# Kernel tuning notes

Measured on AMD Instinct MI355X. Metric: run time of the kernel, lower is better.

## Reference

```python
import jax, jax.numpy as jnp
import numpy as np

N_NODES, N_EDGES, IN_DIM = 100000, 1600000, 64


def setup_inputs() -> dict:
    key = jax.random.key(0)
    k1, k2, k3, k4, k5 = jax.random.split(key, 5)
    h = jax.random.normal(k1, (N_NODES, IN_DIM), dtype=jnp.float32)
    # per-node degree normalizer, e.g. 1/sqrt(deg); positive values in (0,1]
    d = jax.random.uniform(k2, (N_NODES,), dtype=jnp.float32, minval=0.05, maxval=1.0)
    src = jax.random.randint(k3, (N_EDGES,), 0, N_NODES, dtype=jnp.int32)
    dst = jax.random.randint(k4, (N_EDGES,), 0, N_NODES, dtype=jnp.int32)
    # xavier_normal with gain=1.414 for Linear(2*in_dim -> 1)
    xavier_std = 1.414 * np.sqrt(2.0 / (2 * IN_DIM + 1))
    gate_w = jax.random.normal(k5, (1, 2 * IN_DIM), dtype=jnp.float32) * xavier_std
    gate_b = jnp.zeros((1,), dtype=jnp.float32)
    return {"h": h, "d": d, "gate_w": gate_w, "gate_b": gate_b, "src": src, "dst": dst}


def reference(h, d, gate_w, gate_b, src, dst):
    """FAGCN layer forward (dropout in eval mode = identity).

    a_e = tanh(gate([h_dst ; h_src]))        per-edge scalar gate
    e_e = d_dst * d_src * a_e                degree-scaled edge weight
    z_v = sum_{e: dst(e)=v} h_src(e) * e_e   u_mul_e + sum aggregation
    """
    N, D = h.shape
    # gate concat order is [dst, src]; split the [1, 2D] weight so the per-edge
    # GEMV becomes two per-node GEMVs followed by a gather-add (same math).
    w_dst, w_src = gate_w[0, :D], gate_w[0, D:]
    s_dst = h @ w_dst  # [N]
    s_src = h @ w_src  # [N]
    a = jnp.tanh(s_dst[dst] + s_src[src] + gate_b[0])  # [E]
    e = d[dst] * d[src] * a                            # [E] (dropout = identity in eval)
    msg = h[src] * e[:, None]                          # [E, D] gathered messages
    z = jax.ops.segment_sum(msg, dst, num_segments=N)  # [N, D]
    return z
```

## Files before the change

### kernel.cpp

```cpp
#include <hip/hip_runtime.h>

#define D 64
#define NB 2048
#define NPB 49
#define MAXE 1536
#define EPB 2048

__global__ __launch_bounds__(256) void node_phase(
    const float* __restrict__ h,
    const float* __restrict__ deg,
    const float* __restrict__ gate_w,
    const float* __restrict__ gate_b,
    float4* __restrict__ pack,
    int n_nodes)
{
    int gtid = blockIdx.x * blockDim.x + threadIdx.x;
    int node = gtid >> 6;
    int lane = threadIdx.x & 63;
    if (node >= n_nodes) return;

    float hv = h[(size_t)node * D + lane];
    float pd = hv * gate_w[lane];
    float ps = hv * gate_w[D + lane];

    #pragma unroll
    for (int off = 32; off > 0; off >>= 1) {
        pd += __shfl_xor(pd, off);
        ps += __shfl_xor(ps, off);
    }

    if (lane == 0) {
        float4 v;
        v.x = pd + gate_b[0];
        v.y = ps;
        v.z = deg[node];
        v.w = 0.0f;
        pack[node] = v;
    }
}

__global__ __launch_bounds__(256) void bin_hist(
    const int* __restrict__ dst, int* __restrict__ bcount, int n_edges)
{
    __shared__ int cnt[NB];
    for (int i = threadIdx.x; i < NB; i += 256) cnt[i] = 0;
    __syncthreads();
    int stride = gridDim.x * 256;
    for (int e = blockIdx.x * 256 + threadIdx.x; e < n_edges; e += stride)
        atomicAdd(&cnt[(unsigned)dst[e] / NPB], 1);
    __syncthreads();
    for (int i = threadIdx.x; i < NB; i += 256) {
        int c = cnt[i];
        if (c) atomicAdd(&bcount[i], c);
    }
}

__global__ __launch_bounds__(1024) void scan_bases(
    const int* __restrict__ bcount, int* __restrict__ bases,
    int* __restrict__ gcursor, int n_edges)
{
    __shared__ int sm[1024];
    int i0 = 2 * threadIdx.x;
    int a = bcount[i0];
    int b = bcount[i0 + 1];
    int s = a + b;
    sm[threadIdx.x] = s;
    __syncthreads();
    for (int off = 1; off < 1024; off <<= 1) {
        int add = (threadIdx.x >= (unsigned)off) ? sm[threadIdx.x - off] : 0;
        __syncthreads();
        sm[threadIdx.x] += add;
        __syncthreads();
    }
    int excl = sm[threadIdx.x] - s;
    bases[i0]       = excl;
    bases[i0 + 1]   = excl + a;
    gcursor[i0]     = excl;
    gcursor[i0 + 1] = excl + a;
    if (threadIdx.x == 1023) bases[NB] = n_edges;
}

__global__ __launch_bounds__(256) void partition_kernel(
    const int* __restrict__ src, const int* __restrict__ dst,
    const float4* __restrict__ pack, int* __restrict__ gcursor,
    uint2* __restrict__ pairs, int n_edges)
{
    __shared__ int cnt[NB];
    __shared__ int base[NB];
    for (int i = threadIdx.x; i < NB; i += 256) cnt[i] = 0;
    __syncthreads();

    int e0 = blockIdx.x * EPB;
    uint2 payload[8];
    unsigned short bk[8], rk[8];

    #pragma unroll
    for (int k = 0; k < 8; ++k) {
        int e = e0 + k * 256 + threadIdx.x;
        if (e < n_edges) {
            int s = src[e], t = dst[e];
            unsigned b  = (unsigned)t / NPB;
            unsigned dl = (unsigned)t - b * NPB;
            float4 pt = pack[t];
            float4 ps = pack[s];
            float a = tanhf(pt.x + ps.y);
            float w = pt.z * ps.z * a;
            payload[k] = make_uint2((unsigned)s | (dl << 17), __float_as_uint(w));
            bk[k] = (unsigned short)b;
            rk[k] = (unsigned short)atomicAdd(&cnt[b], 1);
        } else {
            bk[k] = 0xFFFF;
        }
    }
    __syncthreads();

    for (int i = threadIdx.x; i < NB; i += 256) {
        int c = cnt[i];
        base[i] = c ? atomicAdd(&gcursor[i], c) : 0;
    }
    __syncthreads();

    #pragma unroll
    for (int k = 0; k < 8; ++k)
        if (bk[k] != 0xFFFF)
            pairs[base[bk[k]] + rk[k]] = payload[k];
}

__global__ __launch_bounds__(256) void bucket_sort_aggregate(
    const float4* __restrict__ h4, const uint2* __restrict__ pairs,
    const int* __restrict__ bases, float* __restrict__ z,
    const float* __restrict__ h, int n_nodes)
{
    __shared__ uint2 lp[MAXE];
    __shared__ unsigned short lidx[MAXE];
    __shared__ int cnt[64], rowbeg[64], cur[64];

    int b     = blockIdx.x;
    int ebeg  = bases[b];
    int eend  = bases[b + 1];
    int total = eend - ebeg;
    int nin   = min(total, MAXE);

    if (threadIdx.x < 64) cnt[threadIdx.x] = 0;
    __syncthreads();

    for (int i = threadIdx.x; i < nin; i += 256) {
        uint2 p = pairs[ebeg + i];
        lp[i] = p;
        atomicAdd(&cnt[p.x >> 17], 1);
    }
    __syncthreads();

    if (threadIdx.x < 64) {
        int v = cnt[threadIdx.x];
        int inc = v;
        #pragma unroll
        for (int off = 1; off < 64; off <<= 1) {
            int t = __shfl_up(inc, off);
            if ((int)threadIdx.x >= off) inc += t;
        }
        rowbeg[threadIdx.x] = inc - v;
        cur[threadIdx.x]    = inc - v;
    }
    __syncthreads();

    for (int i = threadIdx.x; i < nin; i += 256) {
        int dl  = lp[i].x >> 17;
        int pos = atomicAdd(&cur[dl], 1);
        lidx[pos] = (unsigned short)i;
    }
    __syncthreads();

    int wid   = threadIdx.x >> 6;
    int lane  = threadIdx.x & 63;
    int slot  = lane >> 4;
    int chunk = lane & 15;

    for (int n = wid; n < NPB; n += 4) {
        int v = b * NPB + n;
        if (v >= n_nodes) break;
        int rb = rowbeg[n];
        int re = rb + cnt[n];
        float4 acc = make_float4(0.f, 0.f, 0.f, 0.f);
        for (int i = rb + slot; i < re; i += 4) {
            uint2 p = lp[lidx[i]];
            float w = __uint_as_float(p.y);
            float4 hv = h4[(size_t)(p.x & 0x1FFFFu) * (D / 4) + chunk];
            acc.x += hv.x * w;
            acc.y += hv.y * w;
            acc.z += hv.z * w;
            acc.w += hv.w * w;
        }
        #pragma unroll
        for (int off = 16; off <= 32; off <<= 1) {
            acc.x += __shfl_xor(acc.x, off);
            acc.y += __shfl_xor(acc.y, off);
            acc.z += __shfl_xor(acc.z, off);
            acc.w += __shfl_xor(acc.w, off);
        }
        if (slot == 0)
            *(float4*)&z[(size_t)v * D + chunk * 4] = acc;
    }

    if (total > MAXE) {
        __syncthreads();
        for (int i = MAXE + threadIdx.x; i < total; i += 256) {
            uint2 p = pairs[ebeg + i];
            int s  = p.x & 0x1FFFFu;
            int dl = p.x >> 17;
            float w = __uint_as_float(p.y);
            float* zr = z + (size_t)(b * NPB + dl) * D;
            for (int j = 0; j < D; ++j)
                unsafeAtomicAdd(&zr[j], h[(size_t)s * D + j] * w);
        }
    }
}

__global__ __launch_bounds__(256) void edge_phase_atomic(
    const float4* __restrict__ h4,
    const int* __restrict__ src, const int* __restrict__ dst,
    const float4* __restrict__ pack, float* __restrict__ z, int n_edges)
{
    int gtid = blockIdx.x * blockDim.x + threadIdx.x;
    int e_id = gtid >> 4;
    int lane = threadIdx.x & 15;
    if (e_id >= n_edges) return;
    int s = src[e_id], t = dst[e_id];
    float4 pt = pack[t], ps = pack[s];
    float a = tanhf(pt.x + ps.y);
    float e = pt.z * ps.z * a;
    float4 hv = h4[(size_t)s * (D / 4) + lane];
    float* zp = z + (size_t)t * D + lane * 4;
    unsafeAtomicAdd(zp + 0, hv.x * e);
    unsafeAtomicAdd(zp + 1, hv.y * e);
    unsafeAtomicAdd(zp + 2, hv.z * e);
    unsafeAtomicAdd(zp + 3, hv.w * e);
}

extern "C" void kernel_launch(void* const* d_in, const int* in_sizes, int n_in,
                              void* d_out, int out_size, void* d_ws, size_t ws_size,
                              hipStream_t stream)
{
    const float* h   = (const float*)d_in[0];
    const float* deg = (const float*)d_in[1];
    const float* gw  = (const float*)d_in[2];
    const float* gb  = (const float*)d_in[3];
    const int*   src = (const int*)d_in[4];
    const int*   dst = (const int*)d_in[5];

    int n_nodes = in_sizes[1];
    int n_edges = in_sizes[4];

    float* z = (float*)d_out;

    auto align = [](size_t x) { return (x + 255) & ~(size_t)255; };
    size_t pack_b  = align((size_t)n_nodes * sizeof(float4));
    size_t pairs_b = align((size_t)n_edges * sizeof(uint2));
    size_t bcnt_b  = align((size_t)NB * sizeof(int));
    size_t bases_b = align((size_t)(NB + 1) * sizeof(int));
    size_t gcur_b  = align((size_t)NB * sizeof(int));
    size_t need = pack_b + pairs_b + bcnt_b + bases_b + gcur_b;

    char* basep = (char*)d_ws;
    float4* pack    = (float4*)basep;  basep += pack_b;
    uint2*  pairs   = (uint2*)basep;   basep += pairs_b;
    int*    bcount  = (int*)basep;     basep += bcnt_b;
    int*    bases   = (int*)basep;     basep += bases_b;
    int*    gcursor = (int*)basep;

    {
        long long threads = (long long)n_nodes * 64;
        int blocks = (int)((threads + 255) / 256);
        node_phase<<<blocks, 256, 0, stream>>>(h, deg, gw, gb, pack, n_nodes);
    }

    if (ws_size < need || n_nodes > NB * NPB) {
        hipMemsetAsync(d_out, 0, (size_t)n_nodes * D * sizeof(float), stream);
        long long threads = (long long)n_edges * 16;
        int blocks = (int)((threads + 255) / 256);
        edge_phase_atomic<<<blocks, 256, 0, stream>>>((const float4*)h, src, dst, pack, z, n_edges);
        return;
    }

    hipMemsetAsync(bcount, 0, (size_t)NB * sizeof(int), stream);
    bin_hist<<<256, 256, 0, stream>>>(dst, bcount, n_edges);
    scan_bases<<<1, 1024, 0, stream>>>(bcount, bases, gcursor, n_edges);
    {
        int blocks = (n_edges + EPB - 1) / EPB;
        partition_kernel<<<blocks, 256, 0, stream>>>(src, dst, pack, gcursor, pairs, n_edges);
    }
    bucket_sort_aggregate<<<NB, 256, 0, stream>>>(
        (const float4*)h, pairs, bases, z, h, n_nodes);
}
```

Measured before the change: 224.9 us.

## Move edge gate computation into aggregate kernel and shrink partitioned pairs to 4 bytes

The per-edge gate weight is no longer computed in the partition kernel and written alongside the source index. The bucket aggregate kernel now recomputes it: it caches the destination node's pack values in shared memory and gathers pack[src] for each edge. This halves the size of the partitioned pair array, cutting global write and read traffic. The partition kernel also handles twice as many edges per block, which reduces the number of global cursor atomics at the cost of more registers.

```diff
diff --git a/kernel.cpp b/kernel.cpp
--- a/kernel.cpp
+++ b/kernel.cpp
@@ -4,7 +4,7 @@
 #define NB 2048
 #define NPB 49
 #define MAXE 1536
-#define EPB 2048
+#define EPB 4096
 
 __global__ __launch_bounds__(256) void node_phase(
     const float* __restrict__ h,
@@ -82,8 +82,7 @@
 
 __global__ __launch_bounds__(256) void partition_kernel(
     const int* __restrict__ src, const int* __restrict__ dst,
-    const float4* __restrict__ pack, int* __restrict__ gcursor,
-    uint2* __restrict__ pairs, int n_edges)
+    int* __restrict__ gcursor, unsigned* __restrict__ pairs, int n_edges)
 {
     __shared__ int cnt[NB];
     __shared__ int base[NB];
@@ -91,21 +90,17 @@
     __syncthreads();
 
     int e0 = blockIdx.x * EPB;
-    uint2 payload[8];
-    unsigned short bk[8], rk[8];
+    unsigned payload[16];
+    unsigned short bk[16], rk[16];
 
     #pragma unroll
-    for (int k = 0; k < 8; ++k) {
+    for (int k = 0; k < 16; ++k) {
         int e = e0 + k * 256 + threadIdx.x;
         if (e < n_edges) {
             int s = src[e], t = dst[e];
             unsigned b  = (unsigned)t / NPB;
             unsigned dl = (unsigned)t - b * NPB;
-            float4 pt = pack[t];
-            float4 ps = pack[s];
-            float a = tanhf(pt.x + ps.y);
-            float w = pt.z * ps.z * a;
-            payload[k] = make_uint2((unsigned)s | (dl << 17), __float_as_uint(w));
+            payload[k] = (unsigned)s | (dl << 17);
             bk[k] = (unsigned short)b;
             rk[k] = (unsigned short)atomicAdd(&cnt[b], 1);
         } else {
@@ -121,17 +116,19 @@
     __syncthreads();
 
     #pragma unroll
-    for (int k = 0; k < 8; ++k)
+    for (int k = 0; k < 16; ++k)
         if (bk[k] != 0xFFFF)
             pairs[base[bk[k]] + rk[k]] = payload[k];
 }
 
 __global__ __launch_bounds__(256) void bucket_sort_aggregate(
-    const float4* __restrict__ h4, const uint2* __restrict__ pairs,
-    const int* __restrict__ bases, float* __restrict__ z,
-    const float* __restrict__ h, int n_nodes)
-{
-    __shared__ uint2 lp[MAXE];
+    const float4* __restrict__ h4, const unsigned* __restrict__ pairs,
+    const int* __restrict__ bases, const float4* __restrict__ pack,
+    float* __restrict__ z, const float* __restrict__ h, int n_nodes)
+{
+    __shared__ float ptx[NPB], ptz[NPB];
+    __shared__ unsigned lpi[MAXE];
+    __shared__ float    lpw[MAXE];
     __shared__ unsigned short lidx[MAXE];
     __shared__ int cnt[64], rowbeg[64], cur[64];
 
@@ -142,12 +139,25 @@
     int nin   = min(total, MAXE);
 
     if (threadIdx.x < 64) cnt[threadIdx.x] = 0;
+    if (threadIdx.x < NPB) {
+        int v = b * NPB + threadIdx.x;
+        if (v < n_nodes) {
+            float4 p = pack[v];
+            ptx[threadIdx.x] = p.x;
+            ptz[threadIdx.x] = p.z;
+        }
+    }
     __syncthreads();
 
     for (int i = threadIdx.x; i < nin; i += 256) {
-        uint2 p = pairs[ebeg + i];
-        lp[i] = p;
-        atomicAdd(&cnt[p.x >> 17], 1);
+        unsigned p = pairs[ebeg + i];
+        int s  = p & 0x1FFFF;
+        int dl = p >> 17;
+        float4 ps = pack[s];
+        float w = ptz[dl] * ps.z * tanhf(ptx[dl] + ps.y);
+        lpi[i] = p;
+        lpw[i] = w;
+        atomicAdd(&cnt[dl], 1);
     }
     __syncthreads();
 
@@ -165,7 +175,7 @@
     __syncthreads();
 
     for (int i = threadIdx.x; i < nin; i += 256) {
-        int dl  = lp[i].x >> 17;
+        int dl  = lpi[i] >> 17;
         int pos = atomicAdd(&cur[dl], 1);
         lidx[pos] = (unsigned short)i;
     }
@@ -183,9 +193,10 @@
         int re = rb + cnt[n];
         float4 acc = make_float4(0.f, 0.f, 0.f, 0.f);
         for (int i = rb + slot; i < re; i += 4) {
-            uint2 p = lp[lidx[i]];
-            float w = __uint_as_float(p.y);
-            float4 hv = h4[(size_t)(p.x & 0x1FFFFu) * (D / 4) + chunk];
+            int li = lidx[i];
+            unsigned p = lpi[li];
+            float w = lpw[li];
+            float4 hv = h4[(size_t)(p & 0x1FFFFu) * (D / 4) + chunk];
             acc.x += hv.x * w;
             acc.y += hv.y * w;
             acc.z += hv.z * w;
@@ -205,10 +216,11 @@
     if (total > MAXE) {
         __syncthreads();
         for (int i = MAXE + threadIdx.x; i < total; i += 256) {
-            uint2 p = pairs[ebeg + i];
-            int s  = p.x & 0x1FFFFu;
-            int dl = p.x >> 17;
-            float w = __uint_as_float(p.y);
+            unsigned p = pairs[ebeg + i];
+            int s  = p & 0x1FFFF;
+            int dl = p >> 17;
+            float4 ps = pack[s];
+            float w = ptz[dl] * ps.z * tanhf(ptx[dl] + ps.y);
             float* zr = z + (size_t)(b * NPB + dl) * D;
             for (int j = 0; j < D; ++j)
                 unsafeAtomicAdd(&zr[j], h[(size_t)s * D + j] * w);
@@ -255,18 +267,18 @@
 
     auto align = [](size_t x) { return (x + 255) & ~(size_t)255; };
     size_t pack_b  = align((size_t)n_nodes * sizeof(float4));
-    size_t pairs_b = align((size_t)n_edges * sizeof(uint2));
+    size_t pairs_b = align((size_t)n_edges * sizeof(unsigned));
     size_t bcnt_b  = align((size_t)NB * sizeof(int));
     size_t bases_b = align((size_t)(NB + 1) * sizeof(int));
     size_t gcur_b  = align((size_t)NB * sizeof(int));
     size_t need = pack_b + pairs_b + bcnt_b + bases_b + gcur_b;
 
     char* basep = (char*)d_ws;
-    float4* pack    = (float4*)basep;  basep += pack_b;
-    uint2*  pairs   = (uint2*)basep;   basep += pairs_b;
-    int*    bcount  = (int*)basep;     basep += bcnt_b;
-    int*    bases   = (int*)basep;     basep += bases_b;
-    int*    gcursor = (int*)basep;
+    float4*   pack    = (float4*)basep;    basep += pack_b;
+    unsigned* pairs   = (unsigned*)basep;  basep += pairs_b;
+    int*      bcount  = (int*)basep;       basep += bcnt_b;
+    int*      bases   = (int*)basep;       basep += bases_b;
+    int*      gcursor = (int*)basep;
 
     {
         long long threads = (long long)n_nodes * 64;
@@ -287,8 +299,8 @@
     scan_bases<<<1, 1024, 0, stream>>>(bcount, bases, gcursor, n_edges);
     {
         int blocks = (n_edges + EPB - 1) / EPB;
-        partition_kernel<<<blocks, 256, 0, stream>>>(src, dst, pack, gcursor, pairs, n_edges);
+        partition_kernel<<<blocks, 256, 0, stream>>>(src, dst, gcursor, pairs, n_edges);
     }
     bucket_sort_aggregate<<<NB, 256, 0, stream>>>(
-        (const float4*)h, pairs, bases, z, h, n_nodes);
-}
+        (const float4*)h, pairs, bases, pack, z, h, n_nodes);
+}
```

Measured after the change: 207.3 us. 1.08x faster.
